# Kernel tuning notes

Hardware: AMD Instinct MI355X
Metric: run time of the kernel (lower is better)

The kernel has to match this reference:

```python
import jax, jax.numpy as jnp
import numpy as np

N_AZ, N_EL, N_RAD = 4, 2, 2
RADIUS = 0.05
AZ_SCALE = N_AZ / (2.0 * np.pi)
EL_SCALE = N_EL / np.pi


def setup_inputs() -> dict:
    key = jax.random.key(0)
    ks = jax.random.split(key, 7)
    B, N, M, K, C = 4, 8192, 2048, 32, 64
    return {
        "database": jax.random.normal(ks[0], (B, N, 3), dtype=jnp.float32),
        "query": jax.random.normal(ks[1], (B, M, 3), dtype=jnp.float32),
        "nn_index": jax.random.randint(ks[2], (B, M, K), 0, N, dtype=jnp.int64),
        "nn_count": jax.random.randint(ks[3], (B, M), 0, K, dtype=jnp.int32),
        "nn_dist": jax.random.uniform(ks[4], (B, M, K), dtype=jnp.float32),
        "input_features": jax.random.normal(ks[5], (B, N, C), dtype=jnp.float32),
        "filter_weights": jax.random.normal(ks[6], (N_AZ * N_EL * N_RAD, C, 1), dtype=jnp.float32),
    }


def _bins(database, query, nn_index, nn_dist):
    # Gather neighbor coordinates: (B, M, K, 3)
    neighbors = jax.vmap(lambda db, idx: db[idx])(database, nn_index)
    rel = neighbors - query[:, :, None, :]
    x, y, z = rel[..., 0], rel[..., 1], rel[..., 2]
    azimuth = jnp.arctan2(y, x) + np.pi
    elevation = jnp.arccos(jnp.clip(z / (nn_dist + 1e-8), -1.0, 1.0))
    a_bin = azimuth * AZ_SCALE
    e_bin = elevation * EL_SCALE
    r_bin = jnp.clip(nn_dist / RADIUS, 0.0, N_RAD - 1e-6)
    a_fl, e_fl, r_fl = jnp.floor(a_bin), jnp.floor(e_bin), jnp.floor(r_bin)
    a_fr, e_fr, r_fr = a_bin - a_fl, e_bin - e_fl, r_bin - r_fl
    ai, ei, ri = 1.0 - a_fr, 1.0 - e_fr, 1.0 - r_fr
    # 8 trilinear corner coefficients, torch order
    coeff = jnp.stack([
        ai * ei * ri, a_fr * ei * ri, ai * e_fr * ri, a_fr * e_fr * ri,
        ai * ei * r_fr, a_fr * ei * r_fr, ai * e_fr * r_fr, a_fr * e_fr * r_fr,
    ], axis=-1)
    a_fl = a_fl.astype(jnp.int32)
    e_fl = e_fl.astype(jnp.int32)
    r_fl = r_fl.astype(jnp.int32)
    e_c = jnp.clip(e_fl, 0, N_EL - 1)
    e_c1 = jnp.clip(e_fl + 1, 0, N_EL - 1)
    r_c = jnp.clip(r_fl, 0, N_RAD - 1)
    r_c1 = jnp.clip(r_fl + 1, 0, N_RAD - 1)
    base_a = (a_fl % N_AZ) * N_EL
    base_a1 = ((a_fl + 1) % N_AZ) * N_EL
    bin_idx = jnp.stack([
        (base_a + e_c) * N_RAD + r_c, (base_a1 + e_c) * N_RAD + r_c,
        (base_a + e_c1) * N_RAD + r_c, (base_a1 + e_c1) * N_RAD + r_c,
        (base_a + e_c) * N_RAD + r_c1, (base_a1 + e_c) * N_RAD + r_c1,
        (base_a + e_c1) * N_RAD + r_c1, (base_a1 + e_c1) * N_RAD + r_c1,
    ], axis=-1)
    return bin_idx, coeff


def reference(database, query, nn_index, nn_count, nn_dist, input_features, filter_weights):
    bin_idx, coeff = _bins(database, query, nn_index, nn_dist)  # (B,M,K,8)
    # Gather neighbor features: (B, M, K, C)
    nf = jax.vmap(lambda f, idx: f[idx])(input_features, nn_index)
    # filter_weights: (total_bins, C, 1) -> (total_bins, C); gather -> (B,M,K,8,C)
    w = filter_weights[..., 0][bin_idx]
    # Weighted sum over K neighbors and 8 interpolation corners -> (B, M, C)
    out = jnp.einsum('bmkc,bmkec,bmke->bmc', nf, w, coeff)
    return out
```

## Files before the change

### kernel.cpp

```cpp
#include <hip/hip_runtime.h>

#define B_ 4
#define N_ 8192
#define M_ 2048
#define K_ 32
#define C_ 64
#define PTS 8
#define THREADS 256

__device__ __forceinline__ float clampf(float x, float lo, float hi) {
    return fminf(fmaxf(x, lo), hi);
}

__global__ __launch_bounds__(THREADS) void fuzzy_kernel(
    const float* __restrict__ database,
    const float* __restrict__ query,
    const int*   __restrict__ nn_index,
    const float* __restrict__ nn_dist,
    const float* __restrict__ feats,
    const float* __restrict__ filt,
    float*       __restrict__ out)
{
    __shared__ float  Wp[8 * C_ * 2];
    __shared__ float4 c03[PTS][K_];
    __shared__ float4 c47[PTS][K_];
    __shared__ unsigned meta[PTS][K_];

    const int tid = threadIdx.x;

    #pragma unroll
    for (int i = tid; i < 16 * C_; i += THREADS) {
        int t = i >> 6;
        int c = i & 63;
        Wp[(t >> 1) * (C_ * 2) + c * 2 + (t & 1)] = filt[i];
    }

    {
        const int pin = tid >> 5;
        const int k   = tid & 31;
        const int p   = blockIdx.x * PTS + pin;
        const int b   = p >> 11;
        const float qx = query[p * 3 + 0];
        const float qy = query[p * 3 + 1];
        const float qz = query[p * 3 + 2];
        const int   idx  = nn_index[p * K_ + k];
        const float dist = nn_dist[p * K_ + k];
        const int   bidx = b * N_ + idx;
        const float x = database[bidx * 3 + 0] - qx;
        const float y = database[bidx * 3 + 1] - qy;
        const float z = database[bidx * 3 + 2] - qz;

        const float PI_F = 3.14159265358979323846f;
        const float SC   = 0.636619772367581343f;
        float azim = atan2f(y, x) + PI_F;
        float elev = acosf(clampf(z / (dist + 1e-8f), -1.0f, 1.0f));
        float a_bin = azim * SC;
        float e_bin = elev * SC;
        float r_bin = clampf(dist * 20.0f, 0.0f, 1.999999f);
        float a_fl = floorf(a_bin), e_fl = floorf(e_bin), r_fl = floorf(r_bin);
        float a_fr = a_bin - a_fl, e_fr = e_bin - e_fl, r_fr = r_bin - r_fl;
        float ai = 1.0f - a_fr, ei = 1.0f - e_fr, ri = 1.0f - r_fr;
        int a_i = (int)a_fl, e_i = (int)e_fl, r_i = (int)r_fl;
        int a0 = a_i & 3, a1 = (a_i + 1) & 3;
        int ec = e_i < 1 ? e_i : 1;
        unsigned m = (unsigned)(a0 * 2 + ec)
                   | ((unsigned)(a1 * 2 + ec) << 3)
                   | ((unsigned)(a0 * 2 + 1)  << 6)
                   | ((unsigned)(a1 * 2 + 1)  << 9)
                   | ((unsigned)r_i << 12)
                   | ((unsigned)bidx << 13);
        meta[pin][k] = m;
        c03[pin][k] = make_float4(ai * ei * ri,  a_fr * ei * ri,  ai * e_fr * ri,  a_fr * e_fr * ri);
        c47[pin][k] = make_float4(ai * ei * r_fr, a_fr * ei * r_fr, ai * e_fr * r_fr, a_fr * e_fr * r_fr);
    }
    __syncthreads();

    const int wave = tid >> 6;
    const int lane = tid & 63;
    const int pinA = wave * 2;
    const int pinB = pinA + 1;
    const int pA   = blockIdx.x * PTS + pinA;
    float accA = 0.0f, accB = 0.0f;
    const float* WpL = Wp + lane * 2;

    #pragma unroll 8
    for (int k = 0; k < K_; ++k) {
        const unsigned mA = meta[pinA][k];
        const unsigned mB = meta[pinB][k];
        const float4 cA0 = c03[pinA][k];
        const float4 cA1 = c47[pinA][k];
        const float4 cB0 = c03[pinB][k];
        const float4 cB1 = c47[pinB][k];
        const float nfA = feats[((mA >> 13) << 6) + lane];
        const float nfB = feats[((mB >> 13) << 6) + lane];

        {
            const float2 w0 = *(const float2*)(WpL + ((mA      ) & 7u) * 128);
            const float2 w1 = *(const float2*)(WpL + ((mA >> 3 ) & 7u) * 128);
            const float2 w2 = *(const float2*)(WpL + ((mA >> 6 ) & 7u) * 128);
            const float2 w3 = *(const float2*)(WpL + ((mA >> 9 ) & 7u) * 128);
            const bool sr = (mA >> 12) & 1u;
            float e;
            e  = cA0.x * (sr ? w0.y : w0.x) + cA1.x * w0.y;
            e += cA0.y * (sr ? w1.y : w1.x) + cA1.y * w1.y;
            e += cA0.z * (sr ? w2.y : w2.x) + cA1.z * w2.y;
            e += cA0.w * (sr ? w3.y : w3.x) + cA1.w * w3.y;
            accA += nfA * e;
        }
        {
            const float2 w0 = *(const float2*)(WpL + ((mB      ) & 7u) * 128);
            const float2 w1 = *(const float2*)(WpL + ((mB >> 3 ) & 7u) * 128);
            const float2 w2 = *(const float2*)(WpL + ((mB >> 6 ) & 7u) * 128);
            const float2 w3 = *(const float2*)(WpL + ((mB >> 9 ) & 7u) * 128);
            const bool sr = (mB >> 12) & 1u;
            float e;
            e  = cB0.x * (sr ? w0.y : w0.x) + cB1.x * w0.y;
            e += cB0.y * (sr ? w1.y : w1.x) + cB1.y * w1.y;
            e += cB0.z * (sr ? w2.y : w2.x) + cB1.z * w2.y;
            e += cB0.w * (sr ? w3.y : w3.x) + cB1.w * w3.y;
            accB += nfB * e;
        }
    }
    out[pA * C_ + lane]       = accA;
    out[(pA + 1) * C_ + lane] = accB;
}

extern "C" void kernel_launch(void* const* d_in, const int* in_sizes, int n_in,
                              void* d_out, int out_size, void* d_ws, size_t ws_size,
                              hipStream_t stream) {
    const float* database = (const float*)d_in[0];
    const float* query    = (const float*)d_in[1];
    const int*   nn_index = (const int*)d_in[2];
    const float* nn_dist  = (const float*)d_in[4];
    const float* feats    = (const float*)d_in[5];
    const float* filt     = (const float*)d_in[6];
    float* out = (float*)d_out;

    dim3 grid((B_ * M_) / PTS);
    dim3 block(THREADS);
    hipLaunchKernelGGL(fuzzy_kernel, grid, block, 0, stream,
                       database, query, nn_index, nn_dist, feats, filt, out);
}
```

Before: 92.41 us.

## Scatter trilinear coefficients into dense 16-bin weights and keep filter in registers

Each neighbor's 8 trilinear coefficients are now scattered into a dense 16-entry per-bin coefficient vector in shared memory, with elevation and radius clamping folded into the per-axis weights. The inner loop becomes a fixed dot product against the filter column, which each lane now holds in registers as packed float2 pairs. This removes the indexed LDS weight lookups, bit unpacking and selects, and allows packed FMA. In exchange each neighbor reads 64 bytes of coefficients instead of 36, and each thread holds more registers.

```diff
diff --git a/kernel.cpp b/kernel.cpp
--- a/kernel.cpp
+++ b/kernel.cpp
@@ -7,6 +7,9 @@
 #define C_ 64
 #define PTS 8
 #define THREADS 256
+
+typedef float f32x2 __attribute__((ext_vector_type(2)));
+typedef float f32x4 __attribute__((ext_vector_type(4)));
 
 __device__ __forceinline__ float clampf(float x, float lo, float hi) {
     return fminf(fmaxf(x, lo), hi);
@@ -21,18 +24,16 @@
     const float* __restrict__ filt,
     float*       __restrict__ out)
 {
-    __shared__ float  Wp[8 * C_ * 2];
-    __shared__ float4 c03[PTS][K_];
-    __shared__ float4 c47[PTS][K_];
-    __shared__ unsigned meta[PTS][K_];
+    __shared__ f32x4 g[4][PTS][K_];
+    __shared__ int   rowofs[PTS][K_];
 
-    const int tid = threadIdx.x;
+    const int tid  = threadIdx.x;
+    const int lane = tid & 63;
 
+    f32x2 W2[8];
     #pragma unroll
-    for (int i = tid; i < 16 * C_; i += THREADS) {
-        int t = i >> 6;
-        int c = i & 63;
-        Wp[(t >> 1) * (C_ * 2) + c * 2 + (t & 1)] = filt[i];
+    for (int m = 0; m < 8; ++m) {
+        W2[m] = (f32x2){ filt[(2 * m) * C_ + lane], filt[(2 * m + 1) * C_ + lane] };
     }
 
     {
@@ -46,80 +47,61 @@
         const int   idx  = nn_index[p * K_ + k];
         const float dist = nn_dist[p * K_ + k];
         const int   bidx = b * N_ + idx;
+        rowofs[pin][k] = bidx * C_;
         const float x = database[bidx * 3 + 0] - qx;
         const float y = database[bidx * 3 + 1] - qy;
         const float z = database[bidx * 3 + 2] - qz;
 
         const float PI_F = 3.14159265358979323846f;
         const float SC   = 0.636619772367581343f;
-        float azim = atan2f(y, x) + PI_F;
-        float elev = acosf(clampf(z / (dist + 1e-8f), -1.0f, 1.0f));
-        float a_bin = azim * SC;
-        float e_bin = elev * SC;
+        float a_bin = (atan2f(y, x) + PI_F) * SC;
+        float e_bin = acosf(clampf(z / (dist + 1e-8f), -1.0f, 1.0f)) * SC;
         float r_bin = clampf(dist * 20.0f, 0.0f, 1.999999f);
         float a_fl = floorf(a_bin), e_fl = floorf(e_bin), r_fl = floorf(r_bin);
         float a_fr = a_bin - a_fl, e_fr = e_bin - e_fl, r_fr = r_bin - r_fl;
         float ai = 1.0f - a_fr, ei = 1.0f - e_fr, ri = 1.0f - r_fr;
         int a_i = (int)a_fl, e_i = (int)e_fl, r_i = (int)r_fl;
         int a0 = a_i & 3, a1 = (a_i + 1) & 3;
-        int ec = e_i < 1 ? e_i : 1;
-        unsigned m = (unsigned)(a0 * 2 + ec)
-                   | ((unsigned)(a1 * 2 + ec) << 3)
-                   | ((unsigned)(a0 * 2 + 1)  << 6)
-                   | ((unsigned)(a1 * 2 + 1)  << 9)
-                   | ((unsigned)r_i << 12)
-                   | ((unsigned)bidx << 13);
-        meta[pin][k] = m;
-        c03[pin][k] = make_float4(ai * ei * ri,  a_fr * ei * ri,  ai * e_fr * ri,  a_fr * e_fr * ri);
-        c47[pin][k] = make_float4(ai * ei * r_fr, a_fr * ei * r_fr, ai * e_fr * r_fr, a_fr * e_fr * r_fr);
+
+        float E0 = (e_i < 1)  ? ei : 0.0f;
+        float E1 = e_fr + ((e_i >= 1) ? ei : 0.0f);
+        float R0 = (r_i == 0) ? ri : 0.0f;
+        float R1 = r_fr + ((r_i == 1) ? ri : 0.0f);
+        f32x4 er = (f32x4){ E0 * R0, E0 * R1, E1 * R0, E1 * R1 };
+        #pragma unroll
+        for (int j = 0; j < 4; ++j) {
+            float Aj = (j == a0) ? ai : ((j == a1) ? a_fr : 0.0f);
+            g[j][pin][k] = Aj * er;
+        }
     }
     __syncthreads();
 
     const int wave = tid >> 6;
-    const int lane = tid & 63;
     const int pinA = wave * 2;
     const int pinB = pinA + 1;
     const int pA   = blockIdx.x * PTS + pinA;
     float accA = 0.0f, accB = 0.0f;
-    const float* WpL = Wp + lane * 2;
 
     #pragma unroll 8
     for (int k = 0; k < K_; ++k) {
-        const unsigned mA = meta[pinA][k];
-        const unsigned mB = meta[pinB][k];
-        const float4 cA0 = c03[pinA][k];
-        const float4 cA1 = c47[pinA][k];
-        const float4 cB0 = c03[pinB][k];
-        const float4 cB1 = c47[pinB][k];
-        const float nfA = feats[((mA >> 13) << 6) + lane];
-        const float nfB = feats[((mB >> 13) << 6) + lane];
+        const f32x4 gA0 = g[0][pinA][k], gA1 = g[1][pinA][k];
+        const f32x4 gA2 = g[2][pinA][k], gA3 = g[3][pinA][k];
+        const f32x4 gB0 = g[0][pinB][k], gB1 = g[1][pinB][k];
+        const f32x4 gB2 = g[2][pinB][k], gB3 = g[3][pinB][k];
+        const float nfA = feats[rowofs[pinA][k] + lane];
+        const float nfB = feats[rowofs[pinB][k] + lane];
 
-        {
-            const float2 w0 = *(const float2*)(WpL + ((mA      ) & 7u) * 128);
-            const float2 w1 = *(const float2*)(WpL + ((mA >> 3 ) & 7u) * 128);
-            const float2 w2 = *(const float2*)(WpL + ((mA >> 6 ) & 7u) * 128);
-            const float2 w3 = *(const float2*)(WpL + ((mA >> 9 ) & 7u) * 128);
-            const bool sr = (mA >> 12) & 1u;
-            float e;
-            e  = cA0.x * (sr ? w0.y : w0.x) + cA1.x * w0.y;
-            e += cA0.y * (sr ? w1.y : w1.x) + cA1.y * w1.y;
-            e += cA0.z * (sr ? w2.y : w2.x) + cA1.z * w2.y;
-            e += cA0.w * (sr ? w3.y : w3.x) + cA1.w * w3.y;
-            accA += nfA * e;
-        }
-        {
-            const float2 w0 = *(const float2*)(WpL + ((mB      ) & 7u) * 128);
-            const float2 w1 = *(const float2*)(WpL + ((mB >> 3 ) & 7u) * 128);
-            const float2 w2 = *(const float2*)(WpL + ((mB >> 6 ) & 7u) * 128);
-            const float2 w3 = *(const float2*)(WpL + ((mB >> 9 ) & 7u) * 128);
-            const bool sr = (mB >> 12) & 1u;
-            float e;
-            e  = cB0.x * (sr ? w0.y : w0.x) + cB1.x * w0.y;
-            e += cB0.y * (sr ? w1.y : w1.x) + cB1.y * w1.y;
-            e += cB0.z * (sr ? w2.y : w2.x) + cB1.z * w2.y;
-            e += cB0.w * (sr ? w3.y : w3.x) + cB1.w * w3.y;
-            accB += nfB * e;
-        }
+        f32x2 sA = gA0.xy * W2[0] + gA0.zw * W2[1];
+        sA += gA1.xy * W2[2] + gA1.zw * W2[3];
+        sA += gA2.xy * W2[4] + gA2.zw * W2[5];
+        sA += gA3.xy * W2[6] + gA3.zw * W2[7];
+        f32x2 sB = gB0.xy * W2[0] + gB0.zw * W2[1];
+        sB += gB1.xy * W2[2] + gB1.zw * W2[3];
+        sB += gB2.xy * W2[4] + gB2.zw * W2[5];
+        sB += gB3.xy * W2[6] + gB3.zw * W2[7];
+
+        accA += nfA * (sA.x + sA.y);
+        accB += nfB * (sB.x + sB.y);
     }
     out[pA * C_ + lane]       = accA;
     out[(pA + 1) * C_ + lane] = accB;
```

New measurement: 89.72 us. -2.9%, faster.
